# Performance work log

Hardware: AMD Instinct MI355X
Metric: run time of the kernel (lower is better)

## Reference

```python
import jax, jax.numpy as jnp
import numpy as np

B, IN, OUT = 2048, 256, 256

def setup_inputs() -> dict:
    key = jax.random.key(0)
    k1, k2, k3 = jax.random.split(key, 3)
    x = jax.random.normal(k1, (B, IN), dtype=jnp.float32)
    weight = jax.random.normal(k2, (OUT, IN + 1), dtype=jnp.float32)
    w = jax.random.normal(k3, (OUT, IN + 1), dtype=jnp.float32)
    return {"x": x, "weight": weight, "w": w}

def reference(x, weight, w):
    # append bias column of ones: [B, IN+1]
    x_ext = jnp.concatenate([x, jnp.ones((x.shape[0], 1), dtype=x.dtype)], axis=1)
    # y[b,o] = sum_i weight[o,i] * sin(w[o,i] * x_ext[b,i])
    # broadcast to [B, OUT, IN+1], fused sin+mul, reduce over i
    y = jnp.sum(weight[None, :, :] * jnp.sin(w[None, :, :] * x_ext[:, None, :]), axis=2)
    return y
```

## Files before the change

### kernel.cpp

```cpp
#include <hip/hip_runtime.h>


#define IN_DIM 256
#define OUT_DIM 256
#define LDW 257
#define BTILE 8
#define OTILE 16

#define INV_2PI 0.15915494309189535f

__global__ __launch_bounds__(256, 4)
void skan_kernel(const float* __restrict__ x,
                 const float* __restrict__ weight,
                 const float* __restrict__ wfreq,
                 float* __restrict__ y)
{
    const int tid  = threadIdx.x;
    const int lane = tid & 63;
    const int wave = tid >> 6;
    const int iq   = lane & 15;
    const int og   = wave * 4 + (lane >> 4);

    const int obase = (blockIdx.x & 15) * OTILE;
    const int b0    = (blockIdx.x >> 4) * BTILE;
    const int o     = obase + og;

    const float* wr = wfreq  + o * LDW;
    const float* gr = weight + o * LDW;

    float acc[BTILE];
#pragma unroll
    for (int b = 0; b < BTILE; ++b) acc[b] = 0.f;

#pragma unroll
    for (int c = 0; c < 4; ++c) {
        const int i = c * 64 + iq * 4;
        const float w0 = wr[i]     * INV_2PI;
        const float w1 = wr[i + 1] * INV_2PI;
        const float w2 = wr[i + 2] * INV_2PI;
        const float w3 = wr[i + 3] * INV_2PI;
        const float g0 = gr[i], g1 = gr[i + 1], g2 = gr[i + 2], g3 = gr[i + 3];
#pragma unroll
        for (int b = 0; b < BTILE; ++b) {
            const float4 xv = *(const float4*)(x + (b0 + b) * IN_DIM + i);
            float a = acc[b];
            a = fmaf(g0, __builtin_amdgcn_sinf(w0 * xv.x), a);
            a = fmaf(g1, __builtin_amdgcn_sinf(w1 * xv.y), a);
            a = fmaf(g2, __builtin_amdgcn_sinf(w2 * xv.z), a);
            a = fmaf(g3, __builtin_amdgcn_sinf(w3 * xv.w), a);
            acc[b] = a;
        }
    }

    const float bias = gr[IN_DIM] * __builtin_amdgcn_sinf(wr[IN_DIM] * INV_2PI);
    const float sel  = (iq == 0) ? bias : 0.f;
#pragma unroll
    for (int b = 0; b < BTILE; ++b) acc[b] += sel;

#pragma unroll
    for (int b = 0; b < BTILE; ++b) {
        float v = acc[b];
        v += __shfl_xor(v, 1);
        v += __shfl_xor(v, 2);
        v += __shfl_xor(v, 4);
        v += __shfl_xor(v, 8);
        acc[b] = v;
    }

    if (iq == 0) {
#pragma unroll
        for (int b = 0; b < BTILE; ++b) {
            y[(b0 + b) * OUT_DIM + o] = acc[b];
        }
    }
}

extern "C" void kernel_launch(void* const* d_in, const int* in_sizes, int n_in,
                              void* d_out, int out_size, void* d_ws, size_t ws_size,
                              hipStream_t stream) {
    const float* x      = (const float*)d_in[0];
    const float* weight = (const float*)d_in[1];
    const float* wfreq  = (const float*)d_in[2];
    float* y            = (float*)d_out;

    const int B = in_sizes[0] / IN_DIM;
    const int grid = (OUT_DIM / OTILE) * (B / BTILE);

    skan_kernel<<<grid, 256, 0, stream>>>(x, weight, wfreq, y);
}
```

Baseline: 78.90 us.

## Stage weight, frequency and input tiles in LDS before the sin-accumulate loop

Each block now cooperatively loads its 16 weight rows, 16 frequency rows (pre-scaled by 1/2π) and 8 input rows into shared memory with coalesced float4 loads, then runs the inner loop from LDS. This replaces repeated scattered global loads of unaligned stride-257 rows and per-lane x reads. The cost is about 41KB of LDS per block, which forces launch bounds down to 3 blocks per CU and adds a barrier. LDS reads at stride 257 may also cause bank conflicts.

Result: slower. 81.85 us (+3.7%).

```diff
diff --git a/kernel.cpp b/kernel.cpp
--- a/kernel.cpp
+++ b/kernel.cpp
@@ -9,25 +9,51 @@
 
 #define INV_2PI 0.15915494309189535f
 
-__global__ __launch_bounds__(256, 4)
+__global__ __launch_bounds__(256, 3)
 void skan_kernel(const float* __restrict__ x,
                  const float* __restrict__ weight,
                  const float* __restrict__ wfreq,
                  float* __restrict__ y)
 {
-    const int tid  = threadIdx.x;
-    const int lane = tid & 63;
-    const int wave = tid >> 6;
+    __shared__ float lw[OTILE * LDW];
+    __shared__ float lg[OTILE * LDW];
+    __shared__ float lx[BTILE * IN_DIM];
+
+    const int t    = threadIdx.x;
+    const int lane = t & 63;
+    const int wave = t >> 6;
     const int iq   = lane & 15;
     const int og   = wave * 4 + (lane >> 4);
 
     const int obase = (blockIdx.x & 15) * OTILE;
     const int b0    = (blockIdx.x >> 4) * BTILE;
-    const int o     = obase + og;
 
-    const float* wr = wfreq  + o * LDW;
-    const float* gr = weight + o * LDW;
+    {
+        const float4* gw = (const float4*)(wfreq  + obase * LDW);
+        const float4* gg = (const float4*)(weight + obase * LDW);
+        float4* lw4 = (float4*)lw;
+        float4* lg4 = (float4*)lg;
+#pragma unroll
+        for (int k = 0; k < 4; ++k) {
+            float4 v = gw[t + k * 256];
+            v.x *= INV_2PI; v.y *= INV_2PI; v.z *= INV_2PI; v.w *= INV_2PI;
+            lw4[t + k * 256] = v;
+            lg4[t + k * 256] = gg[t + k * 256];
+        }
+        if (t < 4) {
+            float4 v = gw[1024 + t];
+            v.x *= INV_2PI; v.y *= INV_2PI; v.z *= INV_2PI; v.w *= INV_2PI;
+            lw4[1024 + t] = v;
+            lg4[1024 + t] = gg[1024 + t];
+        }
+        const float4* gx = (const float4*)(x + b0 * IN_DIM);
+        float4* lx4 = (float4*)lx;
+        lx4[t]       = gx[t];
+        lx4[t + 256] = gx[t + 256];
+    }
+    __syncthreads();
 
+    const int rw = og * LDW;
     float acc[BTILE];
 #pragma unroll
     for (int b = 0; b < BTILE; ++b) acc[b] = 0.f;
@@ -35,14 +61,13 @@
 #pragma unroll
     for (int c = 0; c < 4; ++c) {
         const int i = c * 64 + iq * 4;
-        const float w0 = wr[i]     * INV_2PI;
-        const float w1 = wr[i + 1] * INV_2PI;
-        const float w2 = wr[i + 2] * INV_2PI;
-        const float w3 = wr[i + 3] * INV_2PI;
-        const float g0 = gr[i], g1 = gr[i + 1], g2 = gr[i + 2], g3 = gr[i + 3];
+        const float w0 = lw[rw + i], w1 = lw[rw + i + 1],
+                    w2 = lw[rw + i + 2], w3 = lw[rw + i + 3];
+        const float g0 = lg[rw + i], g1 = lg[rw + i + 1],
+                    g2 = lg[rw + i + 2], g3 = lg[rw + i + 3];
 #pragma unroll
         for (int b = 0; b < BTILE; ++b) {
-            const float4 xv = *(const float4*)(x + (b0 + b) * IN_DIM + i);
+            const float4 xv = *(const float4*)&lx[b * IN_DIM + i];
             float a = acc[b];
             a = fmaf(g0, __builtin_amdgcn_sinf(w0 * xv.x), a);
             a = fmaf(g1, __builtin_amdgcn_sinf(w1 * xv.y), a);
@@ -52,7 +77,7 @@
         }
     }
 
-    const float bias = gr[IN_DIM] * __builtin_amdgcn_sinf(wr[IN_DIM] * INV_2PI);
+    const float bias = lg[rw + IN_DIM] * __builtin_amdgcn_sinf(lw[rw + IN_DIM]);
     const float sel  = (iq == 0) ? bias : 0.f;
 #pragma unroll
     for (int b = 0; b < BTILE; ++b) acc[b] += sel;
@@ -68,6 +93,7 @@
     }
 
     if (iq == 0) {
+        const int o = obase + og;
 #pragma unroll
         for (int b = 0; b < BTILE; ++b) {
             y[(b0 + b) * OUT_DIM + o] = acc[b];
```
